# Kernel optimization log

Hardware: AMD Instinct MI355X
Metric: run time of the kernel (lower is better)

Reference implementation:

```python
import jax, jax.numpy as jnp
import numpy as np

N_NODE = 50000
N_EDGE = 800000
NODE_DIM, EDGE_DIM = 3, 4


def _relu(x):
    return jnp.maximum(x, 0)


def setup_inputs() -> dict:
    key = jax.random.key(0)
    ks = jax.random.split(key, 32)
    ki = iter(range(32))

    def w(shape):
        fan = shape[0]
        return (jax.random.normal(ks[next(ki)], shape, jnp.float32) / np.float32(np.sqrt(fan)))

    def b(n):
        return jnp.zeros((n,), jnp.float32)

    inp = {
        'nodes': jax.random.normal(ks[next(ki)], (N_NODE, NODE_DIM), jnp.float32),
        'edges': jax.random.normal(ks[next(ki)], (N_EDGE, EDGE_DIM), jnp.float32),
        'senders': jax.random.randint(ks[next(ki)], (N_EDGE,), 0, N_NODE, jnp.int32),
        'receivers': jax.random.randint(ks[next(ki)], (N_EDGE,), 0, N_NODE, jnp.int32),
        # psi1 encoder: [10 -> 256 -> 256 -> 128], relu after every layer (act_final=True)
        'mw0': w((NODE_DIM * 2 + EDGE_DIM, 256)), 'mb0': b(256),
        'mw1': w((256, 256)), 'mb1': b(256),
        'mw2': w((256, 128)), 'mb2': b(128),
        # psi2 attention: [128 -> 128 -> 128 -> 1], no final act
        'aw0': w((128, 128)), 'ab0': b(128),
        'aw1': w((128, 128)), 'ab1': b(128),
        'aw2': w((128, 1)), 'ab2': b(1),
        # psi3 value: [128 -> 256 -> 128], relu after every layer
        'vw0': w((128, 256)), 'vb0': b(256),
        'vw1': w((256, 128)), 'vb1': b(128),
        # psi4 decoder: [128 -> 256 -> 256 -> 1], no final act
        'uw0': w((128, 256)), 'ub0': b(256),
        'uw1': w((256, 256)), 'ub1': b(256),
        'uw2': w((256, 1)), 'ub2': b(1),
    }
    return inp


def reference(nodes, edges, senders, receivers,
              mw0, mb0, mw1, mb1, mw2, mb2,
              aw0, ab0, aw1, ab1, aw2, ab2,
              vw0, vb0, vw1, vb1,
              uw0, ub0, uw1, ub1, uw2, ub2):
    n_node = nodes.shape[0]
    # gather endpoint features and concat with edge features: (E, 2*node_dim+edge_dim)
    z = jnp.concatenate([nodes[senders], nodes[receivers], edges], axis=-1)
    # psi1 encoder (act_final=True)
    q = _relu(_relu(_relu(z @ mw0 + mb0) @ mw1 + mb1) @ mw2 + mb2)  # (E,128)
    # psi2 attention logits (no final act)
    w = (_relu(_relu(q @ aw0 + ab0) @ aw1 + ab1) @ aw2 + ab2)[:, 0]  # (E,)
    # segment softmax over receivers (matches torch scatter_reduce amax with -1e9 init)
    m = jax.ops.segment_max(w, receivers, num_segments=n_node)
    m = jnp.maximum(m, jnp.float32(-1e9))
    ex = jnp.exp(w - m[receivers])
    s = jax.ops.segment_sum(ex, receivers, num_segments=n_node)
    attn = ex / (s[receivers] + 1e-12)  # (E,)
    # psi3 value (act_final=True)
    v = _relu(_relu(q @ vw0 + vb0) @ vw1 + vb1)  # (E,128)
    # attention-weighted scatter-add aggregation to receiver nodes
    aggr = jax.ops.segment_sum(attn[:, None] * v, receivers, num_segments=n_node)  # (N,128)
    # psi4 decoder (no final act)
    out = _relu(_relu(aggr @ uw0 + ub0) @ uw1 + ub1) @ uw2 + ub2  # (N,1)
    return out
```

## Files before the change

kernel.cpp:

```cpp
#include <hip/hip_runtime.h>
#include <stdint.h>

#define NN_NODE 50000
#define NN_EDGE 800000

typedef _Float16 f16;
typedef _Float16 f16x2 __attribute__((ext_vector_type(2)));
typedef _Float16 f16x4 __attribute__((ext_vector_type(4)));
typedef _Float16 f16x8 __attribute__((ext_vector_type(8)));
typedef float f32x4 __attribute__((ext_vector_type(4)));

#define WT_MW0   0
#define WT_MW1   8192
#define WT_MW2   73728
#define WT_AW0   106496
#define WT_AW1   122880
#define WT_VW0   139264
#define WT_VW1   172032
#define WT_UW0   204800
#define WT_UW1   237568
#define WT_TOTAL 303104

#define V_OFF      606208ull
#define WL_OFF     205406208ull
#define CNT_OFF    208606208ull
#define BASE_OFF   208806208ull
#define AGGR_OFF   209006208ull

__device__ __forceinline__ int swz(int row, int col) {
    return row * 256 + ((((col >> 3) ^ (row & 7))) << 3) + (col & 7);
}

template<int K, int N, int NKN, int EPI>
__device__ __forceinline__ void mlayer(const f16* in, int inoff,
        const f16* __restrict__ wt, const float* __restrict__ bias,
        f16* out, int outoff,
        f16x8* bf0, const f16* __restrict__ wtn, f16x8* bfn,
        const float* __restrict__ aw2, float* lpart,
        f16* __restrict__ vout, const int* sposp, int tid)
{
    const int wave = tid >> 6;
    const int lane = tid & 63;
    const int l15  = lane & 15;
    const int quad = lane >> 4;
    constexpr int NKS = K >> 5;
    constexpr int NCT = N >> 4;
    constexpr int ITC = NCT / 4;

    f16x8 af[4][NKS];
#pragma unroll
    for (int ms = 0; ms < 4; ++ms)
#pragma unroll
        for (int ks = 0; ks < NKS; ++ks)
            af[ms][ks] = *(const f16x8*)(in + swz(ms * 16 + l15, inoff + ks * 32 + quad * 8));

    if constexpr (NKN > 0) {
        const f16* wrow = wtn + (size_t)(wave * 16 + l15) * (NKN * 32) + quad * 8;
#pragma unroll
        for (int ks = 0; ks < NKN; ++ks) bfn[ks] = *(const f16x8*)(wrow + ks * 32);
    }

    int   sposv[4];
    float preg[4];
    if constexpr (EPI == 2) {
#pragma unroll
        for (int ms = 0; ms < 4; ++ms) sposv[ms] = sposp[ms * 16 + l15];
    }
    if constexpr (EPI == 1) {
#pragma unroll
        for (int ms = 0; ms < 4; ++ms) preg[ms] = 0.f;
    }

    f16x8 bfl[2][NKS > 0 ? NKS : 1];
#pragma unroll
    for (int ks = 0; ks < NKS; ++ks) bfl[0][ks] = bf0[ks];

#pragma unroll
    for (int i = 0; i < ITC; ++i) {
        const int ct = wave + i * 4;
        if (i + 1 < ITC) {
            const f16* wrow = wt + (size_t)((ct + 4) * 16 + l15) * K + quad * 8;
#pragma unroll
            for (int ks = 0; ks < NKS; ++ks)
                bfl[(i + 1) & 1][ks] = *(const f16x8*)(wrow + ks * 32);
        }
        const int f0 = ct * 16 + quad * 4;
        const float4 bv = *(const float4*)(bias + f0);
        float4 awv;
        if constexpr (EPI == 1) awv = *(const float4*)(aw2 + f0);
#pragma unroll
        for (int ms = 0; ms < 4; ++ms) {
            f32x4 acc = {0.f, 0.f, 0.f, 0.f};
#pragma unroll
            for (int ks = 0; ks < NKS; ++ks)
                acc = __builtin_amdgcn_mfma_f32_16x16x32_f16(bfl[i & 1][ks], af[ms][ks], acc, 0, 0, 0);
            if constexpr (EPI == 0) {
                f16x4 o;
                o[0] = (f16)fmaxf(acc[0] + bv.x, 0.f);
                o[1] = (f16)fmaxf(acc[1] + bv.y, 0.f);
                o[2] = (f16)fmaxf(acc[2] + bv.z, 0.f);
                o[3] = (f16)fmaxf(acc[3] + bv.w, 0.f);
                *(f16x4*)(out + swz(ms * 16 + l15, outoff + f0)) = o;
            } else if constexpr (EPI == 1) {
                preg[ms] += fmaxf(acc[0] + bv.x, 0.f) * awv.x
                          + fmaxf(acc[1] + bv.y, 0.f) * awv.y
                          + fmaxf(acc[2] + bv.z, 0.f) * awv.z
                          + fmaxf(acc[3] + bv.w, 0.f) * awv.w;
            } else {
                f16x4 o;
                o[0] = (f16)fmaxf(acc[0] + bv.x, 0.f);
                o[1] = (f16)fmaxf(acc[1] + bv.y, 0.f);
                o[2] = (f16)fmaxf(acc[2] + bv.z, 0.f);
                o[3] = (f16)fmaxf(acc[3] + bv.w, 0.f);
                *(f16x4*)(vout + (size_t)sposv[ms] * 128 + f0) = o;
            }
        }
    }
    if constexpr (EPI == 1) {
#pragma unroll
        for (int ms = 0; ms < 4; ++ms) {
            float r = preg[ms];
            r += __shfl_xor(r, 16);
            r += __shfl_xor(r, 32);
            if (quad == 0) lpart[wave * 64 + ms * 16 + l15] = r;
        }
    }
}

template<int K, int N>
__device__ __forceinline__ void mfma_layer_basic(const f16* in, int inoff,
        const f16* __restrict__ wt, const float* __restrict__ bias,
        f16* out, int outoff, int tid)
{
    const int wave = tid >> 6;
    const int lane = tid & 63;
    const int l15  = lane & 15;
    const int quad = lane >> 4;
    constexpr int NCT = N >> 4;
    constexpr int NKS = K >> 5;
    f16x8 af[4][NKS];
#pragma unroll
    for (int ms = 0; ms < 4; ++ms)
#pragma unroll
        for (int ks = 0; ks < NKS; ++ks)
            af[ms][ks] = *(const f16x8*)(in + swz(ms * 16 + l15, inoff + ks * 32 + quad * 8));
#pragma unroll 1
    for (int ct = wave; ct < NCT; ct += 4) {
        f16x8 bf[NKS];
        const f16* wrow = wt + (size_t)(ct * 16 + l15) * K + quad * 8;
#pragma unroll
        for (int ks = 0; ks < NKS; ++ks) bf[ks] = *(const f16x8*)(wrow + ks * 32);
        const int f0 = ct * 16 + quad * 4;
        const float4 bv = *(const float4*)(bias + f0);
#pragma unroll
        for (int ms = 0; ms < 4; ++ms) {
            f32x4 acc = {0.f, 0.f, 0.f, 0.f};
#pragma unroll
            for (int ks = 0; ks < NKS; ++ks)
                acc = __builtin_amdgcn_mfma_f32_16x16x32_f16(bf[ks], af[ms][ks], acc, 0, 0, 0);
            f16x4 o;
            o[0] = (f16)fmaxf(acc[0] + bv.x, 0.f);
            o[1] = (f16)fmaxf(acc[1] + bv.y, 0.f);
            o[2] = (f16)fmaxf(acc[2] + bv.z, 0.f);
            o[3] = (f16)fmaxf(acc[3] + bv.w, 0.f);
            *(f16x4*)(out + swz(ms * 16 + l15, outoff + f0)) = o;
        }
    }
}

struct WSeg { const float* src; int K, N, Kpad, dstOff; };
struct WSegs { WSeg s[9]; };

__global__ void prep_kernel(WSegs segs, f16* __restrict__ wt) {
    int idx = blockIdx.x * 256 + threadIdx.x;
    if (idx >= WT_TOTAL) return;
    int off = idx;
#pragma unroll
    for (int i = 0; i < 9; ++i) {
        int sz = segs.s[i].N * segs.s[i].Kpad;
        if (off < sz) {
            int n = off / segs.s[i].Kpad;
            int k = off - n * segs.s[i].Kpad;
            f16 val = (f16)0.f;
            if (k < segs.s[i].K) val = (f16)segs.s[i].src[k * segs.s[i].N + n];
            wt[segs.s[i].dstOff + off] = val;
            return;
        }
        off -= sz;
    }
}

__global__ void hist_kernel(const int* __restrict__ receivers, int* __restrict__ cnt) {
    int e = blockIdx.x * 256 + threadIdx.x;
    atomicAdd(&cnt[receivers[e]], 1);
}

__global__ __launch_bounds__(1024) void scan_kernel(int* __restrict__ cnt, int* __restrict__ base) {
    __shared__ int psum[1024];
    const int tid = threadIdx.x;
    const int CH = (NN_NODE + 1023) / 1024;
    const int lo = tid * CH;
    const int hi = min(lo + CH, NN_NODE);
    int s = 0;
    for (int i = lo; i < hi; ++i) s += cnt[i];
    psum[tid] = s;
    __syncthreads();
    for (int d = 1; d < 1024; d <<= 1) {
        int v = (tid >= d) ? psum[tid - d] : 0;
        __syncthreads();
        psum[tid] += v;
        __syncthreads();
    }
    int run = psum[tid] - s;
    for (int i = lo; i < hi; ++i) {
        int c = cnt[i];
        base[i] = run;
        cnt[i] = run;
        run += c;
    }
}

__global__ __launch_bounds__(256, 2) void edge_kernel(
        const float* __restrict__ nodes, const float* __restrict__ edges,
        const int* __restrict__ senders, const int* __restrict__ receivers,
        const f16* __restrict__ wt,
        const float* __restrict__ mb0, const float* __restrict__ mb1, const float* __restrict__ mb2,
        const float* __restrict__ ab0, const float* __restrict__ ab1,
        const float* __restrict__ aw2, const float* __restrict__ ab2,
        const float* __restrict__ vb0, const float* __restrict__ vb1,
        f16* __restrict__ vout, float* __restrict__ wlog, int* __restrict__ cursor)
{
    __shared__ f16 ldsbuf[2 * 64 * 256];
    __shared__ int spos[64];
    __shared__ float lpart[256];
    f16* bufA = ldsbuf;
    f16* bufB = ldsbuf + 64 * 256;
    const int tid = threadIdx.x;
    const int e0 = blockIdx.x * 64;
    const int wave = tid >> 6;
    const int lane = tid & 63;
    const int l15  = lane & 15;
    const int quad = lane >> 4;

    f16x8 bfA[8], bfB[8];

    {
        const f16* wrow = wt + WT_MW0 + (size_t)(wave * 16 + l15) * 32 + quad * 8;
        bfA[0] = *(const f16x8*)wrow;
    }

    {
        const int e = tid & 63, c = tid >> 6;
        f16x8 zv = {(f16)0.f,(f16)0.f,(f16)0.f,(f16)0.f,(f16)0.f,(f16)0.f,(f16)0.f,(f16)0.f};
        if (c == 0) {
            int s = senders[e0 + e];
            int r = receivers[e0 + e];
            const float2 ev = *(const float2*)(edges + (size_t)(e0 + e) * 4);
            zv[0] = (f16)nodes[s * 3 + 0]; zv[1] = (f16)nodes[s * 3 + 1]; zv[2] = (f16)nodes[s * 3 + 2];
            zv[3] = (f16)nodes[r * 3 + 0]; zv[4] = (f16)nodes[r * 3 + 1]; zv[5] = (f16)nodes[r * 3 + 2];
            zv[6] = (f16)ev.x; zv[7] = (f16)ev.y;
        } else if (c == 1) {
            const float2 ev = *(const float2*)(edges + (size_t)(e0 + e) * 4 + 2);
            zv[0] = (f16)ev.x; zv[1] = (f16)ev.y;
        }
        *(f16x8*)(bufA + e * 256 + ((c ^ (e & 7)) << 3)) = zv;
    }
    __syncthreads();

    mlayer< 32, 256, 8, 0>(bufA, 0, wt + WT_MW0, mb0, bufB, 0, bfA, wt + WT_MW1, bfB,
                           nullptr, nullptr, nullptr, nullptr, tid);
    __syncthreads();
    mlayer<256, 256, 8, 0>(bufB, 0, wt + WT_MW1, mb1, bufA, 0, bfB, wt + WT_MW2, bfA,
                           nullptr, nullptr, nullptr, nullptr, tid);
    __syncthreads();
    mlayer<256, 128, 4, 0>(bufA, 0, wt + WT_MW2, mb2, bufB, 0, bfA, wt + WT_AW0, bfB,
                           nullptr, nullptr, nullptr, nullptr, tid);
    __syncthreads();
    mlayer<128, 128, 4, 0>(bufB, 0, wt + WT_AW0, ab0, bufA, 0, bfB, wt + WT_AW1, bfA,
                           nullptr, nullptr, nullptr, nullptr, tid);
    __syncthreads();
    mlayer<128, 128, 4, 1>(bufA, 0, wt + WT_AW1, ab1, nullptr, 0, bfA, wt + WT_VW0, bfB,
                           aw2, lpart, nullptr, nullptr, tid);
    __syncthreads();

    if (tid < 64) {
        float wv = lpart[tid] + lpart[64 + tid] + lpart[128 + tid] + lpart[192 + tid] + ab2[0];
        int r = receivers[e0 + tid];
        int pos = atomicAdd(&cursor[r], 1);
        spos[tid] = pos;
        wlog[pos] = wv;
    }
    mlayer<128, 256, 8, 0>(bufB, 0, wt + WT_VW0, vb0, bufA, 0, bfB, wt + WT_VW1, bfA,
                           nullptr, nullptr, nullptr, nullptr, tid);
    __syncthreads();
    mlayer<256, 128, 0, 2>(bufA, 0, wt + WT_VW1, vb1, nullptr, 0, bfA, nullptr, nullptr,
                           nullptr, nullptr, vout, spos, tid);
}

__global__ __launch_bounds__(256) void aggregate_kernel(
        const float* __restrict__ wlog, const f16* __restrict__ v,
        const int* __restrict__ base, float* __restrict__ aggr)
{
    const int tid = threadIdx.x;
    const int n = blockIdx.x * 4 + (tid >> 6);
    const int lane = tid & 63;
    const int st = base[n];
    const int en = (n == NN_NODE - 1) ? NN_EDGE : base[n + 1];

    float mx = -1e9f;
    for (int i = st + lane; i < en; i += 64) mx = fmaxf(mx, wlog[i]);
#pragma unroll
    for (int d = 1; d < 64; d <<= 1) mx = fmaxf(mx, __shfl_xor(mx, d));

    float sm = 0.f;
    for (int i = st + lane; i < en; i += 64) sm += __expf(wlog[i] - mx);
#pragma unroll
    for (int d = 1; d < 64; d <<= 1) sm += __shfl_xor(sm, d);
    const float inv = 1.f / (sm + 1e-12f);

    float acc0 = 0.f, acc1 = 0.f;
    const f16* vp = v + (size_t)st * 128 + lane * 2;
    for (int i = st; i < en; ++i, vp += 128) {
        float attn = __expf(wlog[i] - mx) * inv;
        f16x2 vv = *(const f16x2*)vp;
        acc0 += attn * (float)vv[0];
        acc1 += attn * (float)vv[1];
    }
    float2 o; o.x = acc0; o.y = acc1;
    *(float2*)(aggr + (size_t)n * 128 + lane * 2) = o;
}

__global__ __launch_bounds__(256, 2) void node_kernel(
        const float* __restrict__ aggr, const f16* __restrict__ wt,
        const float* __restrict__ ub0, const float* __restrict__ ub1,
        const float* __restrict__ uw2, const float* __restrict__ ub2,
        float* __restrict__ out)
{
    __shared__ f16 ldsbuf[2 * 64 * 256];
    f16* bufA = ldsbuf;
    f16* bufB = ldsbuf + 64 * 256;
    const int tid = threadIdx.x;
    const int n0 = blockIdx.x * 64;
    {
        int row = tid >> 2, j = tid & 3;
        int n = n0 + row;
        if (n < NN_NODE) {
            const float4* src = (const float4*)(aggr + (size_t)n * 128 + j * 32);
#pragma unroll
            for (int i = 0; i < 8; ++i) {
                float4 t4 = src[i];
                int c = j * 32 + i * 4;
                bufA[swz(row, c + 0)] = (f16)t4.x;
                bufA[swz(row, c + 1)] = (f16)t4.y;
                bufA[swz(row, c + 2)] = (f16)t4.z;
                bufA[swz(row, c + 3)] = (f16)t4.w;
            }
        } else {
#pragma unroll
            for (int i = 0; i < 32; ++i) bufA[swz(row, j * 32 + i)] = (f16)0.f;
        }
    }
    __syncthreads();
    mfma_layer_basic<128, 256>(bufA, 0, wt + WT_UW0, ub0, bufB, 0, tid); __syncthreads();
    mfma_layer_basic<256, 256>(bufB, 0, wt + WT_UW1, ub1, bufA, 0, tid); __syncthreads();
    {
        int e = tid >> 2, part = tid & 3;
        float sum = 0.f;
        for (int c = part * 64; c < part * 64 + 64; ++c)
            sum += (float)bufA[swz(e, c)] * uw2[c];
        sum += __shfl_down(sum, 2);
        sum += __shfl_down(sum, 1);
        int n = n0 + e;
        if (part == 0 && n < NN_NODE) out[n] = sum + ub2[0];
    }
}

extern "C" void kernel_launch(void* const* d_in, const int* in_sizes, int n_in,
                              void* d_out, int out_size, void* d_ws, size_t ws_size,
                              hipStream_t stream)
{
    const float* nodes     = (const float*)d_in[0];
    const float* edges     = (const float*)d_in[1];
    const int*   senders   = (const int*)d_in[2];
    const int*   receivers = (const int*)d_in[3];
    const float* mw0 = (const float*)d_in[4];  const float* mb0 = (const float*)d_in[5];
    const float* mw1 = (const float*)d_in[6];  const float* mb1 = (const float*)d_in[7];
    const float* mw2 = (const float*)d_in[8];  const float* mb2 = (const float*)d_in[9];
    const float* aw0 = (const float*)d_in[10]; const float* ab0 = (const float*)d_in[11];
    const float* aw1 = (const float*)d_in[12]; const float* ab1 = (const float*)d_in[13];
    const float* aw2 = (const float*)d_in[14]; const float* ab2 = (const float*)d_in[15];
    const float* vw0 = (const float*)d_in[16]; const float* vb0 = (const float*)d_in[17];
    const float* vw1 = (const float*)d_in[18]; const float* vb1 = (const float*)d_in[19];
    const float* uw0 = (const float*)d_in[20]; const float* ub0 = (const float*)d_in[21];
    const float* uw1 = (const float*)d_in[22]; const float* ub1 = (const float*)d_in[23];
    const float* uw2 = (const float*)d_in[24]; const float* ub2 = (const float*)d_in[25];

    char* ws = (char*)d_ws;
    f16*   wt   = (f16*)ws;
    f16*   vbuf = (f16*)(ws + V_OFF);
    float* wlog = (float*)(ws + WL_OFF);
    int*   cnt  = (int*)(ws + CNT_OFF);
    int*   base = (int*)(ws + BASE_OFF);
    float* aggr = (float*)(ws + AGGR_OFF);
    float* out  = (float*)d_out;

    hipMemsetAsync(cnt, 0, NN_NODE * sizeof(int), stream);

    WSegs segs = {{
        { mw0,  10, 256,  32, WT_MW0 },
        { mw1, 256, 256, 256, WT_MW1 },
        { mw2, 256, 128, 256, WT_MW2 },
        { aw0, 128, 128, 128, WT_AW0 },
        { aw1, 128, 128, 128, WT_AW1 },
        { vw0, 128, 256, 128, WT_VW0 },
        { vw1, 256, 128, 256, WT_VW1 },
        { uw0, 128, 256, 128, WT_UW0 },
        { uw1, 256, 256, 256, WT_UW1 },
    }};
    prep_kernel<<<(WT_TOTAL + 255) / 256, 256, 0, stream>>>(segs, wt);

    hist_kernel<<<NN_EDGE / 256, 256, 0, stream>>>(receivers, cnt);
    scan_kernel<<<1, 1024, 0, stream>>>(cnt, base);

    edge_kernel<<<NN_EDGE / 64, 256, 0, stream>>>(nodes, edges, senders, receivers, wt,
        mb0, mb1, mb2, ab0, ab1, aw2, ab2, vb0, vb1, vbuf, wlog, cnt);

    aggregate_kernel<<<NN_NODE / 4, 256, 0, stream>>>(wlog, vbuf, base, aggr);

    node_kernel<<<(NN_NODE + 63) / 64, 256, 0, stream>>>(aggr, wt, ub0, ub1, uw2, ub2, out);
}
```

Baseline: 990.4 us.

## Split K dimension into halves in MFMA layers to cut register pressure

The MLP layer routine now walks the K dimension in chunks of at most 128 and keeps all output-tile accumulators live across the chunks, so the A fragments and weight prefetch buffers hold only half of K. The next-layer weight prefetch shrinks to the first K chunk. This lowers vector register use, which could raise occupancy or stop spilling. In exchange it keeps more accumulator registers live and reloads the weight rows for each K chunk.

```diff
diff --git a/kernel.cpp b/kernel.cpp
--- a/kernel.cpp
+++ b/kernel.cpp
@@ -31,7 +31,7 @@
     return row * 256 + ((((col >> 3) ^ (row & 7))) << 3) + (col & 7);
 }
 
-template<int K, int N, int NKN, int EPI>
+template<int K, int N, int KN, int EPI>
 __device__ __forceinline__ void mlayer(const f16* in, int inoff,
         const f16* __restrict__ wt, const float* __restrict__ bias,
         f16* out, int outoff,
@@ -43,75 +43,112 @@
     const int lane = tid & 63;
     const int l15  = lane & 15;
     const int quad = lane >> 4;
-    constexpr int NKS = K >> 5;
-    constexpr int NCT = N >> 4;
-    constexpr int ITC = NCT / 4;
-
-    f16x8 af[4][NKS];
-#pragma unroll
-    for (int ms = 0; ms < 4; ++ms)
-#pragma unroll
-        for (int ks = 0; ks < NKS; ++ks)
-            af[ms][ks] = *(const f16x8*)(in + swz(ms * 16 + l15, inoff + ks * 32 + quad * 8));
-
-    if constexpr (NKN > 0) {
-        const f16* wrow = wtn + (size_t)(wave * 16 + l15) * (NKN * 32) + quad * 8;
-#pragma unroll
-        for (int ks = 0; ks < NKN; ++ks) bfn[ks] = *(const f16x8*)(wrow + ks * 32);
-    }
-
-    int   sposv[4];
+    constexpr int NKS  = K >> 5;
+    constexpr int NKH  = (NKS > 4) ? 4 : NKS;
+    constexpr int NH   = NKS / NKH;
+    constexpr int NCT  = N >> 4;
+    constexpr int ITC  = NCT / 4;
+    constexpr int NKNH = (KN >= 128) ? 4 : (KN >> 5);
+
+    f32x4 acc[ITC][4];
+#pragma unroll
+    for (int i = 0; i < ITC; ++i)
+#pragma unroll
+        for (int ms = 0; ms < 4; ++ms)
+            acc[i][ms] = (f32x4){0.f, 0.f, 0.f, 0.f};
+
+    int sposv[4];
+    if constexpr (EPI == 2) {
+#pragma unroll
+        for (int ms = 0; ms < 4; ++ms) sposv[ms] = sposp[ms * 16 + l15];
+    }
+
+    f16x8 bfl[2][NKH];
+
+#pragma unroll
+    for (int h = 0; h < NH; ++h) {
+        if (h == 0) {
+#pragma unroll
+            for (int ks = 0; ks < NKH; ++ks) bfl[0][ks] = bf0[ks];
+        } else {
+            const f16* wrow = wt + (size_t)(wave * 16 + l15) * K + h * NKH * 32 + quad * 8;
+#pragma unroll
+            for (int ks = 0; ks < NKH; ++ks)
+                bfl[0][ks] = *(const f16x8*)(wrow + ks * 32);
+        }
+
+        f16x8 af[4][NKH];
+#pragma unroll
+        for (int ms = 0; ms < 4; ++ms)
+#pragma unroll
+            for (int ks = 0; ks < NKH; ++ks)
+                af[ms][ks] = *(const f16x8*)(in + swz(ms * 16 + l15,
+                                    inoff + (h * NKH + ks) * 32 + quad * 8));
+#pragma unroll
+        for (int ms = 0; ms < 4; ++ms)
+#pragma unroll
+            for (int ks = 0; ks < NKH; ++ks)
+                asm volatile("" : "+v"(af[ms][ks]));
+
+        if constexpr (KN > 0) {
+            if (h == NH - 1) {
+                const f16* wrow = wtn + (size_t)(wave * 16 + l15) * KN + quad * 8;
+#pragma unroll
+                for (int ks = 0; ks < NKNH; ++ks)
+                    bfn[ks] = *(const f16x8*)(wrow + ks * 32);
+            }
+        }
+
+#pragma unroll
+        for (int i = 0; i < ITC; ++i) {
+            const int ct = wave + i * 4;
+            if (i + 1 < ITC) {
+                const f16* wrow2 = wt + (size_t)((ct + 4) * 16 + l15) * K + h * NKH * 32 + quad * 8;
+#pragma unroll
+                for (int ks = 0; ks < NKH; ++ks)
+                    bfl[(i + 1) & 1][ks] = *(const f16x8*)(wrow2 + ks * 32);
+            }
+#pragma unroll
+            for (int ms = 0; ms < 4; ++ms)
+#pragma unroll
+                for (int ks = 0; ks < NKH; ++ks)
+                    acc[i][ms] = __builtin_amdgcn_mfma_f32_16x16x32_f16(
+                        bfl[i & 1][ks], af[ms][ks], acc[i][ms], 0, 0, 0);
+        }
+    }
+
     float preg[4];
-    if constexpr (EPI == 2) {
-#pragma unroll
-        for (int ms = 0; ms < 4; ++ms) sposv[ms] = sposp[ms * 16 + l15];
-    }
     if constexpr (EPI == 1) {
 #pragma unroll
         for (int ms = 0; ms < 4; ++ms) preg[ms] = 0.f;
     }
-
-    f16x8 bfl[2][NKS > 0 ? NKS : 1];
-#pragma unroll
-    for (int ks = 0; ks < NKS; ++ks) bfl[0][ks] = bf0[ks];
-
 #pragma unroll
     for (int i = 0; i < ITC; ++i) {
         const int ct = wave + i * 4;
-        if (i + 1 < ITC) {
-            const f16* wrow = wt + (size_t)((ct + 4) * 16 + l15) * K + quad * 8;
-#pragma unroll
-            for (int ks = 0; ks < NKS; ++ks)
-                bfl[(i + 1) & 1][ks] = *(const f16x8*)(wrow + ks * 32);
-        }
         const int f0 = ct * 16 + quad * 4;
         const float4 bv = *(const float4*)(bias + f0);
         float4 awv;
         if constexpr (EPI == 1) awv = *(const float4*)(aw2 + f0);
 #pragma unroll
         for (int ms = 0; ms < 4; ++ms) {
-            f32x4 acc = {0.f, 0.f, 0.f, 0.f};
-#pragma unroll
-            for (int ks = 0; ks < NKS; ++ks)
-                acc = __builtin_amdgcn_mfma_f32_16x16x32_f16(bfl[i & 1][ks], af[ms][ks], acc, 0, 0, 0);
             if constexpr (EPI == 0) {
                 f16x4 o;
-                o[0] = (f16)fmaxf(acc[0] + bv.x, 0.f);
-                o[1] = (f16)fmaxf(acc[1] + bv.y, 0.f);
-                o[2] = (f16)fmaxf(acc[2] + bv.z, 0.f);
-                o[3] = (f16)fmaxf(acc[3] + bv.w, 0.f);
+                o[0] = (f16)fmaxf(acc[i][ms][0] + bv.x, 0.f);
+                o[1] = (f16)fmaxf(acc[i][ms][1] + bv.y, 0.f);
+                o[2] = (f16)fmaxf(acc[i][ms][2] + bv.z, 0.f);
+                o[3] = (f16)fmaxf(acc[i][ms][3] + bv.w, 0.f);
                 *(f16x4*)(out + swz(ms * 16 + l15, outoff + f0)) = o;
             } else if constexpr (EPI == 1) {
-                preg[ms] += fmaxf(acc[0] + bv.x, 0.f) * awv.x
-                          + fmaxf(acc[1] + bv.y, 0.f) * awv.y
-                          + fmaxf(acc[2] + bv.z, 0.f) * awv.z
-                          + fmaxf(acc[3] + bv.w, 0.f) * awv.w;
+                preg[ms] += fmaxf(acc[i][ms][0] + bv.x, 0.f) * awv.x
+                          + fmaxf(acc[i][ms][1] + bv.y, 0.f) * awv.y
+                          + fmaxf(acc[i][ms][2] + bv.z, 0.f) * awv.z
+                          + fmaxf(acc[i][ms][3] + bv.w, 0.f) * awv.w;
             } else {
                 f16x4 o;
-                o[0] = (f16)fmaxf(acc[0] + bv.x, 0.f);
-                o[1] = (f16)fmaxf(acc[1] + bv.y, 0.f);
-                o[2] = (f16)fmaxf(acc[2] + bv.z, 0.f);
-                o[3] = (f16)fmaxf(acc[3] + bv.w, 0.f);
+                o[0] = (f16)fmaxf(acc[i][ms][0] + bv.x, 0.f);
+                o[1] = (f16)fmaxf(acc[i][ms][1] + bv.y, 0.f);
+                o[2] = (f16)fmaxf(acc[i][ms][2] + bv.z, 0.f);
+                o[3] = (f16)fmaxf(acc[i][ms][3] + bv.w, 0.f);
                 *(f16x4*)(vout + (size_t)sposv[ms] * 128 + f0) = o;
             }
         }
@@ -242,7 +279,7 @@
     const int l15  = lane & 15;
     const int quad = lane >> 4;
 
-    f16x8 bfA[8], bfB[8];
+    f16x8 bfA[4], bfB[4];
 
     {
         const f16* wrow = wt + WT_MW0 + (size_t)(wave * 16 + l15) * 32 + quad * 8;
@@ -267,20 +304,20 @@
     }
     __syncthreads();
 
-    mlayer< 32, 256, 8, 0>(bufA, 0, wt + WT_MW0, mb0, bufB, 0, bfA, wt + WT_MW1, bfB,
-                           nullptr, nullptr, nullptr, nullptr, tid);
-    __syncthreads();
-    mlayer<256, 256, 8, 0>(bufB, 0, wt + WT_MW1, mb1, bufA, 0, bfB, wt + WT_MW2, bfA,
-                           nullptr, nullptr, nullptr, nullptr, tid);
-    __syncthreads();
-    mlayer<256, 128, 4, 0>(bufA, 0, wt + WT_MW2, mb2, bufB, 0, bfA, wt + WT_AW0, bfB,
-                           nullptr, nullptr, nullptr, nullptr, tid);
-    __syncthreads();
-    mlayer<128, 128, 4, 0>(bufB, 0, wt + WT_AW0, ab0, bufA, 0, bfB, wt + WT_AW1, bfA,
-                           nullptr, nullptr, nullptr, nullptr, tid);
-    __syncthreads();
-    mlayer<128, 128, 4, 1>(bufA, 0, wt + WT_AW1, ab1, nullptr, 0, bfA, wt + WT_VW0, bfB,
-                           aw2, lpart, nullptr, nullptr, tid);
+    mlayer< 32, 256, 256, 0>(bufA, 0, wt + WT_MW0, mb0, bufB, 0, bfA, wt + WT_MW1, bfB,
+                             nullptr, nullptr, nullptr, nullptr, tid);
+    __syncthreads();
+    mlayer<256, 256, 256, 0>(bufB, 0, wt + WT_MW1, mb1, bufA, 0, bfB, wt + WT_MW2, bfA,
+                             nullptr, nullptr, nullptr, nullptr, tid);
+    __syncthreads();
+    mlayer<256, 128, 128, 0>(bufA, 0, wt + WT_MW2, mb2, bufB, 0, bfA, wt + WT_AW0, bfB,
+                             nullptr, nullptr, nullptr, nullptr, tid);
+    __syncthreads();
+    mlayer<128, 128, 128, 0>(bufB, 0, wt + WT_AW0, ab0, bufA, 0, bfB, wt + WT_AW1, bfA,
+                             nullptr, nullptr, nullptr, nullptr, tid);
+    __syncthreads();
+    mlayer<128, 128, 128, 1>(bufA, 0, wt + WT_AW1, ab1, nullptr, 0, bfA, wt + WT_VW0, bfB,
+                             aw2, lpart, nullptr, nullptr, tid);
     __syncthreads();
 
     if (tid < 64) {
@@ -290,8 +327,8 @@
         spos[tid] = pos;
         wlog[pos] = wv;
     }
-    mlayer<128, 256, 8, 0>(bufB, 0, wt + WT_VW0, vb0, bufA, 0, bfB, wt + WT_VW1, bfA,
-                           nullptr, nullptr, nullptr, nullptr, tid);
+    mlayer<128, 256, 256, 0>(bufB, 0, wt + WT_VW0, vb0, bufA, 0, bfB, wt + WT_VW1, bfA,
+                             nullptr, nullptr, nullptr, nullptr, tid);
     __syncthreads();
     mlayer<256, 128, 0, 2>(bufA, 0, wt + WT_VW1, vb1, nullptr, 0, bfA, nullptr, nullptr,
                            nullptr, nullptr, vout, spos, tid);
```

Result: no change. 973.7 us (-1.7%).

## Make each wave compute the full edge MLP chain independently without block barriers

Applied to the files above, without the earlier changes.

The edge kernel becomes 128-thread blocks in which each wave owns 32 edges, holds its own LDS tile, and computes every output column of each layer. This removes the `__syncthreads` between layers and the LDS exchange of attention partial sums and scatter positions; the logit reduction and atomic slot allocation now use wave shuffles. Accumulators are initialised with the bias, and the K dimension is processed in halves with double-buffered weight fragments. In exchange, each weight matrix is streamed from global or L2 once per 32 edges instead of once per 64, doubling weight traffic. Each weight fragment also feeds only two MFMA row tiles instead of four, and the large accumulator arrays raise register pressure.

```diff
diff --git a/kernel.cpp b/kernel.cpp
--- a/kernel.cpp
+++ b/kernel.cpp
@@ -31,98 +31,120 @@
     return row * 256 + ((((col >> 3) ^ (row & 7))) << 3) + (col & 7);
 }
 
-template<int K, int N, int NKN, int EPI>
-__device__ __forceinline__ void mlayer(const f16* in, int inoff,
+template<int K, int N, int EPI>
+__device__ __forceinline__ void mlayerW(f16* sl, int inoff, int outoff,
         const f16* __restrict__ wt, const float* __restrict__ bias,
-        f16* out, int outoff,
-        f16x8* bf0, const f16* __restrict__ wtn, f16x8* bfn,
-        const float* __restrict__ aw2, float* lpart,
-        f16* __restrict__ vout, const int* sposp, int tid)
-{
-    const int wave = tid >> 6;
-    const int lane = tid & 63;
+        const float* __restrict__ aw2, const float* __restrict__ ab2,
+        float* __restrict__ wlog, int* __restrict__ cursor,
+        const int* __restrict__ receivers, int e0w,
+        f16* __restrict__ vout, int& pos, int lane)
+{
     const int l15  = lane & 15;
     const int quad = lane >> 4;
     constexpr int NKS = K >> 5;
+    constexpr int NKH = (NKS > 4) ? 4 : NKS;
+    constexpr int NH  = NKS / NKH;
     constexpr int NCT = N >> 4;
-    constexpr int ITC = NCT / 4;
-
-    f16x8 af[4][NKS];
-#pragma unroll
-    for (int ms = 0; ms < 4; ++ms)
-#pragma unroll
-        for (int ks = 0; ks < NKS; ++ks)
-            af[ms][ks] = *(const f16x8*)(in + swz(ms * 16 + l15, inoff + ks * 32 + quad * 8));
-
-    if constexpr (NKN > 0) {
-        const f16* wrow = wtn + (size_t)(wave * 16 + l15) * (NKN * 32) + quad * 8;
-#pragma unroll
-        for (int ks = 0; ks < NKN; ++ks) bfn[ks] = *(const f16x8*)(wrow + ks * 32);
-    }
-
-    int   sposv[4];
-    float preg[4];
-    if constexpr (EPI == 2) {
-#pragma unroll
-        for (int ms = 0; ms < 4; ++ms) sposv[ms] = sposp[ms * 16 + l15];
-    }
-    if constexpr (EPI == 1) {
-#pragma unroll
-        for (int ms = 0; ms < 4; ++ms) preg[ms] = 0.f;
-    }
-
-    f16x8 bfl[2][NKS > 0 ? NKS : 1];
-#pragma unroll
-    for (int ks = 0; ks < NKS; ++ks) bfl[0][ks] = bf0[ks];
-
-#pragma unroll
-    for (int i = 0; i < ITC; ++i) {
-        const int ct = wave + i * 4;
-        if (i + 1 < ITC) {
-            const f16* wrow = wt + (size_t)((ct + 4) * 16 + l15) * K + quad * 8;
-#pragma unroll
-            for (int ks = 0; ks < NKS; ++ks)
-                bfl[(i + 1) & 1][ks] = *(const f16x8*)(wrow + ks * 32);
-        }
-        const int f0 = ct * 16 + quad * 4;
-        const float4 bv = *(const float4*)(bias + f0);
-        float4 awv;
-        if constexpr (EPI == 1) awv = *(const float4*)(aw2 + f0);
-#pragma unroll
-        for (int ms = 0; ms < 4; ++ms) {
-            f32x4 acc = {0.f, 0.f, 0.f, 0.f};
-#pragma unroll
-            for (int ks = 0; ks < NKS; ++ks)
-                acc = __builtin_amdgcn_mfma_f32_16x16x32_f16(bfl[i & 1][ks], af[ms][ks], acc, 0, 0, 0);
-            if constexpr (EPI == 0) {
+
+    f32x4 acc[NCT][2];
+#pragma unroll
+    for (int ct = 0; ct < NCT; ++ct) {
+        const float4 bv = *(const float4*)(bias + ct * 16 + quad * 4);
+        f32x4 a = {bv.x, bv.y, bv.z, bv.w};
+        acc[ct][0] = a;
+        acc[ct][1] = a;
+    }
+
+    f16x8 W[2][NKH];
+    f16x8 af[2][NKH];
+
+#pragma unroll
+    for (int h = 0; h < NH; ++h) {
+#pragma unroll
+        for (int m = 0; m < 2; ++m)
+#pragma unroll
+            for (int ks = 0; ks < NKH; ++ks)
+                af[m][ks] = *(const f16x8*)(sl + swz(m * 16 + l15,
+                                    inoff + (h * NKH + ks) * 32 + quad * 8));
+#pragma unroll
+        for (int m = 0; m < 2; ++m)
+#pragma unroll
+            for (int ks = 0; ks < NKH; ++ks)
+                asm volatile("" : "+v"(af[m][ks]));
+
+#pragma unroll
+        for (int t = 0; t < 2; ++t) {
+            const f16* wr = wt + (size_t)(t * 16 + l15) * K + h * NKH * 32 + quad * 8;
+#pragma unroll
+            for (int ks = 0; ks < NKH; ++ks) W[t][ks] = *(const f16x8*)(wr + ks * 32);
+        }
+#pragma unroll
+        for (int ct = 0; ct < NCT; ++ct) {
+#pragma unroll
+            for (int m = 0; m < 2; ++m)
+#pragma unroll
+                for (int ks = 0; ks < NKH; ++ks)
+                    acc[ct][m] = __builtin_amdgcn_mfma_f32_16x16x32_f16(
+                        W[ct & 1][ks], af[m][ks], acc[ct][m], 0, 0, 0);
+            if (ct + 2 < NCT) {
+                const f16* wr = wt + (size_t)((ct + 2) * 16 + l15) * K + h * NKH * 32 + quad * 8;
+#pragma unroll
+                for (int ks = 0; ks < NKH; ++ks) W[ct & 1][ks] = *(const f16x8*)(wr + ks * 32);
+            }
+        }
+    }
+
+    if constexpr (EPI == 0) {
+#pragma unroll
+        for (int ct = 0; ct < NCT; ++ct) {
+            const int f0 = ct * 16 + quad * 4;
+#pragma unroll
+            for (int m = 0; m < 2; ++m) {
                 f16x4 o;
-                o[0] = (f16)fmaxf(acc[0] + bv.x, 0.f);
-                o[1] = (f16)fmaxf(acc[1] + bv.y, 0.f);
-                o[2] = (f16)fmaxf(acc[2] + bv.z, 0.f);
-                o[3] = (f16)fmaxf(acc[3] + bv.w, 0.f);
-                *(f16x4*)(out + swz(ms * 16 + l15, outoff + f0)) = o;
-            } else if constexpr (EPI == 1) {
-                preg[ms] += fmaxf(acc[0] + bv.x, 0.f) * awv.x
-                          + fmaxf(acc[1] + bv.y, 0.f) * awv.y
-                          + fmaxf(acc[2] + bv.z, 0.f) * awv.z
-                          + fmaxf(acc[3] + bv.w, 0.f) * awv.w;
-            } else {
-                f16x4 o;
-                o[0] = (f16)fmaxf(acc[0] + bv.x, 0.f);
-                o[1] = (f16)fmaxf(acc[1] + bv.y, 0.f);
-                o[2] = (f16)fmaxf(acc[2] + bv.z, 0.f);
-                o[3] = (f16)fmaxf(acc[3] + bv.w, 0.f);
-                *(f16x4*)(vout + (size_t)sposv[ms] * 128 + f0) = o;
+                o[0] = (f16)fmaxf(acc[ct][m][0], 0.f);
+                o[1] = (f16)fmaxf(acc[ct][m][1], 0.f);
+                o[2] = (f16)fmaxf(acc[ct][m][2], 0.f);
+                o[3] = (f16)fmaxf(acc[ct][m][3], 0.f);
+                *(f16x4*)(sl + swz(m * 16 + l15, outoff + f0)) = o;
             }
         }
-    }
-    if constexpr (EPI == 1) {
-#pragma unroll
-        for (int ms = 0; ms < 4; ++ms) {
-            float r = preg[ms];
-            r += __shfl_xor(r, 16);
-            r += __shfl_xor(r, 32);
-            if (quad == 0) lpart[wave * 64 + ms * 16 + l15] = r;
+    } else if constexpr (EPI == 1) {
+        float p0 = 0.f, p1 = 0.f;
+#pragma unroll
+        for (int ct = 0; ct < NCT; ++ct) {
+            const float4 awv = *(const float4*)(aw2 + ct * 16 + quad * 4);
+            p0 += fmaxf(acc[ct][0][0], 0.f) * awv.x + fmaxf(acc[ct][0][1], 0.f) * awv.y
+                + fmaxf(acc[ct][0][2], 0.f) * awv.z + fmaxf(acc[ct][0][3], 0.f) * awv.w;
+            p1 += fmaxf(acc[ct][1][0], 0.f) * awv.x + fmaxf(acc[ct][1][1], 0.f) * awv.y
+                + fmaxf(acc[ct][1][2], 0.f) * awv.z + fmaxf(acc[ct][1][3], 0.f) * awv.w;
+        }
+        p0 += __shfl_xor(p0, 16); p0 += __shfl_xor(p0, 32);
+        p1 += __shfl_xor(p1, 16); p1 += __shfl_xor(p1, 32);
+        pos = 0;
+        if (quad < 2) {
+            float lg = (quad == 0 ? p0 : p1) + ab2[0];
+            int ge = e0w + quad * 16 + l15;
+            int r = receivers[ge];
+            pos = atomicAdd(&cursor[r], 1);
+            wlog[pos] = lg;
+        }
+    } else {
+        const int s0 = __shfl(pos, l15);
+        const int s1 = __shfl(pos, 16 + l15);
+#pragma unroll
+        for (int ct = 0; ct < NCT; ++ct) {
+            const int f0 = ct * 16 + quad * 4;
+            f16x4 o0, o1;
+            o0[0] = (f16)fmaxf(acc[ct][0][0], 0.f);
+            o0[1] = (f16)fmaxf(acc[ct][0][1], 0.f);
+            o0[2] = (f16)fmaxf(acc[ct][0][2], 0.f);
+            o0[3] = (f16)fmaxf(acc[ct][0][3], 0.f);
+            o1[0] = (f16)fmaxf(acc[ct][1][0], 0.f);
+            o1[1] = (f16)fmaxf(acc[ct][1][1], 0.f);
+            o1[2] = (f16)fmaxf(acc[ct][1][2], 0.f);
+            o1[3] = (f16)fmaxf(acc[ct][1][3], 0.f);
+            *(f16x4*)(vout + (size_t)s0 * 128 + f0) = o0;
+            *(f16x4*)(vout + (size_t)s1 * 128 + f0) = o1;
         }
     }
 }
@@ -220,7 +242,7 @@
     }
 }
 
-__global__ __launch_bounds__(256, 2) void edge_kernel(
+__global__ __launch_bounds__(128, 2) void edge_kernel(
         const float* __restrict__ nodes, const float* __restrict__ edges,
         const int* __restrict__ senders, const int* __restrict__ receivers,
         const f16* __restrict__ wt,
@@ -230,71 +252,55 @@
         const float* __restrict__ vb0, const float* __restrict__ vb1,
         f16* __restrict__ vout, float* __restrict__ wlog, int* __restrict__ cursor)
 {
-    __shared__ f16 ldsbuf[2 * 64 * 256];
-    __shared__ int spos[64];
-    __shared__ float lpart[256];
-    f16* bufA = ldsbuf;
-    f16* bufB = ldsbuf + 64 * 256;
-    const int tid = threadIdx.x;
-    const int e0 = blockIdx.x * 64;
+    __shared__ f16 buf[2 * 32 * 256];
+    const int tid  = threadIdx.x;
     const int wave = tid >> 6;
     const int lane = tid & 63;
-    const int l15  = lane & 15;
-    const int quad = lane >> 4;
-
-    f16x8 bfA[8], bfB[8];
+    f16* sl = buf + wave * 32 * 256;
+    const int e0w = blockIdx.x * 64 + wave * 32;
 
     {
-        const f16* wrow = wt + WT_MW0 + (size_t)(wave * 16 + l15) * 32 + quad * 8;
-        bfA[0] = *(const f16x8*)wrow;
-    }
-
-    {
-        const int e = tid & 63, c = tid >> 6;
-        f16x8 zv = {(f16)0.f,(f16)0.f,(f16)0.f,(f16)0.f,(f16)0.f,(f16)0.f,(f16)0.f,(f16)0.f};
-        if (c == 0) {
-            int s = senders[e0 + e];
-            int r = receivers[e0 + e];
-            const float2 ev = *(const float2*)(edges + (size_t)(e0 + e) * 4);
-            zv[0] = (f16)nodes[s * 3 + 0]; zv[1] = (f16)nodes[s * 3 + 1]; zv[2] = (f16)nodes[s * 3 + 2];
-            zv[3] = (f16)nodes[r * 3 + 0]; zv[4] = (f16)nodes[r * 3 + 1]; zv[5] = (f16)nodes[r * 3 + 2];
-            zv[6] = (f16)ev.x; zv[7] = (f16)ev.y;
-        } else if (c == 1) {
-            const float2 ev = *(const float2*)(edges + (size_t)(e0 + e) * 4 + 2);
-            zv[0] = (f16)ev.x; zv[1] = (f16)ev.y;
-        }
-        *(f16x8*)(bufA + e * 256 + ((c ^ (e & 7)) << 3)) = zv;
-    }
-    __syncthreads();
-
-    mlayer< 32, 256, 8, 0>(bufA, 0, wt + WT_MW0, mb0, bufB, 0, bfA, wt + WT_MW1, bfB,
-                           nullptr, nullptr, nullptr, nullptr, tid);
-    __syncthreads();
-    mlayer<256, 256, 8, 0>(bufB, 0, wt + WT_MW1, mb1, bufA, 0, bfB, wt + WT_MW2, bfA,
-                           nullptr, nullptr, nullptr, nullptr, tid);
-    __syncthreads();
-    mlayer<256, 128, 4, 0>(bufA, 0, wt + WT_MW2, mb2, bufB, 0, bfA, wt + WT_AW0, bfB,
-                           nullptr, nullptr, nullptr, nullptr, tid);
-    __syncthreads();
-    mlayer<128, 128, 4, 0>(bufB, 0, wt + WT_AW0, ab0, bufA, 0, bfB, wt + WT_AW1, bfA,
-                           nullptr, nullptr, nullptr, nullptr, tid);
-    __syncthreads();
-    mlayer<128, 128, 4, 1>(bufA, 0, wt + WT_AW1, ab1, nullptr, 0, bfA, wt + WT_VW0, bfB,
-                           aw2, lpart, nullptr, nullptr, tid);
-    __syncthreads();
-
-    if (tid < 64) {
-        float wv = lpart[tid] + lpart[64 + tid] + lpart[128 + tid] + lpart[192 + tid] + ab2[0];
-        int r = receivers[e0 + tid];
-        int pos = atomicAdd(&cursor[r], 1);
-        spos[tid] = pos;
-        wlog[pos] = wv;
-    }
-    mlayer<128, 256, 8, 0>(bufB, 0, wt + WT_VW0, vb0, bufA, 0, bfB, wt + WT_VW1, bfA,
-                           nullptr, nullptr, nullptr, nullptr, tid);
-    __syncthreads();
-    mlayer<256, 128, 0, 2>(bufA, 0, wt + WT_VW1, vb1, nullptr, 0, bfA, nullptr, nullptr,
-                           nullptr, nullptr, vout, spos, tid);
+        const int er = lane & 31;
+        const int g  = lane >> 5;
+        f16x8 c0 = {(f16)0.f,(f16)0.f,(f16)0.f,(f16)0.f,(f16)0.f,(f16)0.f,(f16)0.f,(f16)0.f};
+        f16x8 c1 = c0;
+        if (g == 0) {
+            int ge = e0w + er;
+            int s = senders[ge];
+            int r = receivers[ge];
+            const float2 ev0 = *(const float2*)(edges + (size_t)ge * 4);
+            const float2 ev1 = *(const float2*)(edges + (size_t)ge * 4 + 2);
+            c0[0] = (f16)nodes[s * 3 + 0]; c0[1] = (f16)nodes[s * 3 + 1]; c0[2] = (f16)nodes[s * 3 + 2];
+            c0[3] = (f16)nodes[r * 3 + 0]; c0[4] = (f16)nodes[r * 3 + 1]; c0[5] = (f16)nodes[r * 3 + 2];
+            c0[6] = (f16)ev0.x; c0[7] = (f16)ev0.y;
+            c1[0] = (f16)ev1.x; c1[1] = (f16)ev1.y;
+        }
+        *(f16x8*)(sl + er * 256 + (((2 * g + 0) ^ (er & 7)) << 3)) = c0;
+        *(f16x8*)(sl + er * 256 + (((2 * g + 1) ^ (er & 7)) << 3)) = c1;
+    }
+    asm volatile("" ::: "memory");
+
+    int pos = 0;
+    mlayerW< 32, 256, 0>(sl, 0, 0, wt + WT_MW0, mb0, nullptr, nullptr,
+                         nullptr, nullptr, nullptr, 0, nullptr, pos, lane);
+    asm volatile("" ::: "memory");
+    mlayerW<256, 256, 0>(sl, 0, 0, wt + WT_MW1, mb1, nullptr, nullptr,
+                         nullptr, nullptr, nullptr, 0, nullptr, pos, lane);
+    asm volatile("" ::: "memory");
+    mlayerW<256, 128, 0>(sl, 0, 0, wt + WT_MW2, mb2, nullptr, nullptr,
+                         nullptr, nullptr, nullptr, 0, nullptr, pos, lane);
+    asm volatile("" ::: "memory");
+    mlayerW<128, 128, 0>(sl, 0, 128, wt + WT_AW0, ab0, nullptr, nullptr,
+                         nullptr, nullptr, nullptr, 0, nullptr, pos, lane);
+    asm volatile("" ::: "memory");
+    mlayerW<128, 128, 1>(sl, 128, 0, wt + WT_AW1, ab1, aw2, ab2,
+                         wlog, cursor, receivers, e0w, nullptr, pos, lane);
+    asm volatile("" ::: "memory");
+    mlayerW<128, 256, 0>(sl, 0, 0, wt + WT_VW0, vb0, nullptr, nullptr,
+                         nullptr, nullptr, nullptr, 0, nullptr, pos, lane);
+    asm volatile("" ::: "memory");
+    mlayerW<256, 128, 2>(sl, 0, 0, wt + WT_VW1, vb1, nullptr, nullptr,
+                         nullptr, nullptr, nullptr, 0, vout, pos, lane);
 }
 
 __global__ __launch_bounds__(256) void aggregate_kernel(
@@ -422,7 +428,7 @@
     hist_kernel<<<NN_EDGE / 256, 256, 0, stream>>>(receivers, cnt);
     scan_kernel<<<1, 1024, 0, stream>>>(cnt, base);
 
-    edge_kernel<<<NN_EDGE / 64, 256, 0, stream>>>(nodes, edges, senders, receivers, wt,
+    edge_kernel<<<NN_EDGE / 64, 128, 0, stream>>>(nodes, edges, senders, receivers, wt,
         mb0, mb1, mb2, ab0, ab1, aw2, ab2, vb0, vb1, vbuf, wlog, cnt);
 
     aggregate_kernel<<<NN_NODE / 4, 256, 0, stream>>>(wlog, vbuf, base, aggr);
```

Result: slower. 1.611 ms (+62.7%).

## Restructure edge MLP into K-chunked accumulation with single in-place LDS buffer

Applied to the files above, without the earlier changes.

Replaces the per-layer full-K A-fragment load plus cross-layer weight prefetch with a K-chunked loop that keeps all output-column accumulators in registers. Each layer now reads and writes one shared 64x256 LDS buffer in place, with an internal barrier before overwriting its input. Halving LDS and cutting register pressure allows raising launch bounds from 2 to 4 blocks per SIMD to improve occupancy. The cost is extra barriers, weight loads no longer prefetched across layers, and more accumulator registers per thread.

```diff
diff --git a/kernel.cpp b/kernel.cpp
--- a/kernel.cpp
+++ b/kernel.cpp
@@ -31,11 +31,9 @@
     return row * 256 + ((((col >> 3) ^ (row & 7))) << 3) + (col & 7);
 }
 
-template<int K, int N, int NKN, int EPI>
-__device__ __forceinline__ void mlayer(const f16* in, int inoff,
+template<int K, int N, int EPI, int IBAR>
+__device__ __forceinline__ void mlayerR(f16* buf, int inoff, int outoff,
         const f16* __restrict__ wt, const float* __restrict__ bias,
-        f16* out, int outoff,
-        f16x8* bf0, const f16* __restrict__ wtn, f16x8* bfn,
         const float* __restrict__ aw2, float* lpart,
         f16* __restrict__ vout, const int* sposp, int tid)
 {
@@ -43,86 +41,99 @@
     const int lane = tid & 63;
     const int l15  = lane & 15;
     const int quad = lane >> 4;
-    constexpr int NKS = K >> 5;
-    constexpr int NCT = N >> 4;
-    constexpr int ITC = NCT / 4;
-
-    f16x8 af[4][NKS];
-#pragma unroll
-    for (int ms = 0; ms < 4; ++ms)
-#pragma unroll
-        for (int ks = 0; ks < NKS; ++ks)
-            af[ms][ks] = *(const f16x8*)(in + swz(ms * 16 + l15, inoff + ks * 32 + quad * 8));
-
-    if constexpr (NKN > 0) {
-        const f16* wrow = wtn + (size_t)(wave * 16 + l15) * (NKN * 32) + quad * 8;
-#pragma unroll
-        for (int ks = 0; ks < NKN; ++ks) bfn[ks] = *(const f16x8*)(wrow + ks * 32);
-    }
-
-    int   sposv[4];
+    constexpr int KS = (K >= 64) ? 2 : 1;
+    constexpr int KC = KS * 32;
+    constexpr int NC = K / KC;
+    constexpr int C  = (N >> 4) / 4;
+
+    f32x4 acc[C][4];
+#pragma unroll
+    for (int ci = 0; ci < C; ++ci)
+#pragma unroll
+        for (int m = 0; m < 4; ++m)
+            acc[ci][m] = (f32x4){0.f, 0.f, 0.f, 0.f};
+
+#pragma unroll 1
+    for (int kc = 0; kc < NC; ++kc) {
+        f16x8 af[4][KS];
+#pragma unroll
+        for (int m = 0; m < 4; ++m)
+#pragma unroll
+            for (int ks = 0; ks < KS; ++ks)
+                af[m][ks] = *(const f16x8*)(buf + swz(m * 16 + l15,
+                                    inoff + kc * KC + ks * 32 + quad * 8));
+#pragma unroll
+        for (int m = 0; m < 4; ++m)
+#pragma unroll
+            for (int ks = 0; ks < KS; ++ks)
+                asm volatile("" : "+v"(af[m][ks]));
+
+#pragma unroll
+        for (int ci = 0; ci < C; ++ci) {
+            const int ct = wave + ci * 4;
+            f16x8 W[KS];
+            const f16* wr = wt + (size_t)(ct * 16 + l15) * K + kc * KC + quad * 8;
+#pragma unroll
+            for (int ks = 0; ks < KS; ++ks) W[ks] = *(const f16x8*)(wr + ks * 32);
+#pragma unroll
+            for (int m = 0; m < 4; ++m)
+#pragma unroll
+                for (int ks = 0; ks < KS; ++ks)
+                    acc[ci][m] = __builtin_amdgcn_mfma_f32_16x16x32_f16(
+                        W[ks], af[m][ks], acc[ci][m], 0, 0, 0);
+        }
+    }
+
+    if constexpr (IBAR) __syncthreads();
+
     float preg[4];
+    if constexpr (EPI == 1) {
+#pragma unroll
+        for (int m = 0; m < 4; ++m) preg[m] = 0.f;
+    }
+    int sposv[4];
     if constexpr (EPI == 2) {
 #pragma unroll
-        for (int ms = 0; ms < 4; ++ms) sposv[ms] = sposp[ms * 16 + l15];
-    }
-    if constexpr (EPI == 1) {
-#pragma unroll
-        for (int ms = 0; ms < 4; ++ms) preg[ms] = 0.f;
-    }
-
-    f16x8 bfl[2][NKS > 0 ? NKS : 1];
-#pragma unroll
-    for (int ks = 0; ks < NKS; ++ks) bfl[0][ks] = bf0[ks];
-
-#pragma unroll
-    for (int i = 0; i < ITC; ++i) {
-        const int ct = wave + i * 4;
-        if (i + 1 < ITC) {
-            const f16* wrow = wt + (size_t)((ct + 4) * 16 + l15) * K + quad * 8;
-#pragma unroll
-            for (int ks = 0; ks < NKS; ++ks)
-                bfl[(i + 1) & 1][ks] = *(const f16x8*)(wrow + ks * 32);
-        }
+        for (int m = 0; m < 4; ++m) sposv[m] = sposp[m * 16 + l15];
+    }
+#pragma unroll
+    for (int ci = 0; ci < C; ++ci) {
+        const int ct = wave + ci * 4;
         const int f0 = ct * 16 + quad * 4;
         const float4 bv = *(const float4*)(bias + f0);
         float4 awv;
         if constexpr (EPI == 1) awv = *(const float4*)(aw2 + f0);
 #pragma unroll
-        for (int ms = 0; ms < 4; ++ms) {
-            f32x4 acc = {0.f, 0.f, 0.f, 0.f};
-#pragma unroll
-            for (int ks = 0; ks < NKS; ++ks)
-                acc = __builtin_amdgcn_mfma_f32_16x16x32_f16(bfl[i & 1][ks], af[ms][ks], acc, 0, 0, 0);
+        for (int m = 0; m < 4; ++m) {
             if constexpr (EPI == 0) {
                 f16x4 o;
-                o[0] = (f16)fmaxf(acc[0] + bv.x, 0.f);
-                o[1] = (f16)fmaxf(acc[1] + bv.y, 0.f);
-                o[2] = (f16)fmaxf(acc[2] + bv.z, 0.f);
-                o[3] = (f16)fmaxf(acc[3] + bv.w, 0.f);
-                *(f16x4*)(out + swz(ms * 16 + l15, outoff + f0)) = o;
+                o[0] = (f16)fmaxf(acc[ci][m][0] + bv.x, 0.f);
+                o[1] = (f16)fmaxf(acc[ci][m][1] + bv.y, 0.f);
+                o[2] = (f16)fmaxf(acc[ci][m][2] + bv.z, 0.f);
+                o[3] = (f16)fmaxf(acc[ci][m][3] + bv.w, 0.f);
+                *(f16x4*)(buf + swz(m * 16 + l15, outoff + f0)) = o;
             } else if constexpr (EPI == 1) {
-                preg[ms] += fmaxf(acc[0] + bv.x, 0.f) * awv.x
-                          + fmaxf(acc[1] + bv.y, 0.f) * awv.y
-                          + fmaxf(acc[2] + bv.z, 0.f) * awv.z
-                          + fmaxf(acc[3] + bv.w, 0.f) * awv.w;
+                preg[m] += fmaxf(acc[ci][m][0] + bv.x, 0.f) * awv.x
+                         + fmaxf(acc[ci][m][1] + bv.y, 0.f) * awv.y
+                         + fmaxf(acc[ci][m][2] + bv.z, 0.f) * awv.z
+                         + fmaxf(acc[ci][m][3] + bv.w, 0.f) * awv.w;
             } else {
                 f16x4 o;
-                o[0] = (f16)fmaxf(acc[0] + bv.x, 0.f);
-                o[1] = (f16)fmaxf(acc[1] + bv.y, 0.f);
-                o[2] = (f16)fmaxf(acc[2] + bv.z, 0.f);
-                o[3] = (f16)fmaxf(acc[3] + bv.w, 0.f);
-                *(f16x4*)(vout + (size_t)sposv[ms] * 128 + f0) = o;
+                o[0] = (f16)fmaxf(acc[ci][m][0] + bv.x, 0.f);
+                o[1] = (f16)fmaxf(acc[ci][m][1] + bv.y, 0.f);
+                o[2] = (f16)fmaxf(acc[ci][m][2] + bv.z, 0.f);
+                o[3] = (f16)fmaxf(acc[ci][m][3] + bv.w, 0.f);
+                *(f16x4*)(vout + (size_t)sposv[m] * 128 + f0) = o;
             }
         }
     }
     if constexpr (EPI == 1) {
 #pragma unroll
-        for (int ms = 0; ms < 4; ++ms) {
-            float r = preg[ms];
+        for (int m = 0; m < 4; ++m) {
+            float r = preg[m];
             r += __shfl_xor(r, 16);
             r += __shfl_xor(r, 32);
-            if (quad == 0) lpart[wave * 64 + ms * 16 + l15] = r;
+            if (quad == 0) lpart[wave * 64 + m * 16 + l15] = r;
         }
     }
 }
@@ -220,7 +231,7 @@
     }
 }
 
-__global__ __launch_bounds__(256, 2) void edge_kernel(
+__global__ __launch_bounds__(256, 4) void edge_kernel(
         const float* __restrict__ nodes, const float* __restrict__ edges,
         const int* __restrict__ senders, const int* __restrict__ receivers,
         const f16* __restrict__ wt,
@@ -230,24 +241,11 @@
         const float* __restrict__ vb0, const float* __restrict__ vb1,
         f16* __restrict__ vout, float* __restrict__ wlog, int* __restrict__ cursor)
 {
-    __shared__ f16 ldsbuf[2 * 64 * 256];
+    __shared__ f16 buf[64 * 256];
     __shared__ int spos[64];
     __shared__ float lpart[256];
-    f16* bufA = ldsbuf;
-    f16* bufB = ldsbuf + 64 * 256;
     const int tid = threadIdx.x;
     const int e0 = blockIdx.x * 64;
-    const int wave = tid >> 6;
-    const int lane = tid & 63;
-    const int l15  = lane & 15;
-    const int quad = lane >> 4;
-
-    f16x8 bfA[8], bfB[8];
-
-    {
-        const f16* wrow = wt + WT_MW0 + (size_t)(wave * 16 + l15) * 32 + quad * 8;
-        bfA[0] = *(const f16x8*)wrow;
-    }
 
     {
         const int e = tid & 63, c = tid >> 6;
@@ -263,24 +261,19 @@
             const float2 ev = *(const float2*)(edges + (size_t)(e0 + e) * 4 + 2);
             zv[0] = (f16)ev.x; zv[1] = (f16)ev.y;
         }
-        *(f16x8*)(bufA + e * 256 + ((c ^ (e & 7)) << 3)) = zv;
-    }
-    __syncthreads();
-
-    mlayer< 32, 256, 8, 0>(bufA, 0, wt + WT_MW0, mb0, bufB, 0, bfA, wt + WT_MW1, bfB,
-                           nullptr, nullptr, nullptr, nullptr, tid);
-    __syncthreads();
-    mlayer<256, 256, 8, 0>(bufB, 0, wt + WT_MW1, mb1, bufA, 0, bfB, wt + WT_MW2, bfA,
-                           nullptr, nullptr, nullptr, nullptr, tid);
-    __syncthreads();
-    mlayer<256, 128, 4, 0>(bufA, 0, wt + WT_MW2, mb2, bufB, 0, bfA, wt + WT_AW0, bfB,
-                           nullptr, nullptr, nullptr, nullptr, tid);
-    __syncthreads();
-    mlayer<128, 128, 4, 0>(bufB, 0, wt + WT_AW0, ab0, bufA, 0, bfB, wt + WT_AW1, bfA,
-                           nullptr, nullptr, nullptr, nullptr, tid);
-    __syncthreads();
-    mlayer<128, 128, 4, 1>(bufA, 0, wt + WT_AW1, ab1, nullptr, 0, bfA, wt + WT_VW0, bfB,
-                           aw2, lpart, nullptr, nullptr, tid);
+        *(f16x8*)(buf + e * 256 + ((c ^ (e & 7)) << 3)) = zv;
+    }
+    __syncthreads();
+
+    mlayerR< 32, 256, 0, 1>(buf, 0, 0, wt + WT_MW0, mb0, nullptr, nullptr, nullptr, nullptr, tid);
+    __syncthreads();
+    mlayerR<256, 256, 0, 1>(buf, 0, 0, wt + WT_MW1, mb1, nullptr, nullptr, nullptr, nullptr, tid);
+    __syncthreads();
+    mlayerR<256, 128, 0, 1>(buf, 0, 0, wt + WT_MW2, mb2, nullptr, nullptr, nullptr, nullptr, tid);
+    __syncthreads();
+    mlayerR<128, 128, 0, 0>(buf, 0, 128, wt + WT_AW0, ab0, nullptr, nullptr, nullptr, nullptr, tid);
+    __syncthreads();
+    mlayerR<128, 128, 1, 0>(buf, 128, 0, wt + WT_AW1, ab1, aw2, lpart, nullptr, nullptr, tid);
     __syncthreads();
 
     if (tid < 64) {
@@ -290,11 +283,9 @@
         spos[tid] = pos;
         wlog[pos] = wv;
     }
-    mlayer<128, 256, 8, 0>(bufB, 0, wt + WT_VW0, vb0, bufA, 0, bfB, wt + WT_VW1, bfA,
-                           nullptr, nullptr, nullptr, nullptr, tid);
-    __syncthreads();
-    mlayer<256, 128, 0, 2>(bufA, 0, wt + WT_VW1, vb1, nullptr, 0, bfA, nullptr, nullptr,
-                           nullptr, nullptr, vout, spos, tid);
+    mlayerR<128, 256, 0, 1>(buf, 0, 0, wt + WT_VW0, vb0, nullptr, nullptr, nullptr, nullptr, tid);
+    __syncthreads();
+    mlayerR<256, 128, 2, 0>(buf, 0, 0, wt + WT_VW1, vb1, nullptr, nullptr, vout, spos, tid);
 }
 
 __global__ __launch_bounds__(256) void aggregate_kernel(
```

New measurement: 976.3 us. No clear change (-1.4%).
